# Kernel tuning notes

Hardware: AMD Instinct MI355X
Metric: run time of the kernel (lower is better)

## Reference

```python
import jax, jax.numpy as jnp
import numpy as np

STEP = 0.01  # matches init kwarg step=0.01


def _disc(x, step=STEP):
    """Discretize like pd.cut with bins arange(floor(min), ceil(max)+step, step).
    Bin identity is all that matters for entropy, so we return integer bin ids.
    (Boundary convention: half-open floor binning; pd.cut uses right-closed,
    which differs only on exact bin edges - measure-zero for continuous data.)"""
    lower = jnp.floor(jnp.min(x))
    return jnp.floor((x - lower) / step).astype(jnp.int32)


def _row_joint_entropy(labels_list):
    """Per-row empirical (joint) entropy in nats of discrete label tuples.
    H_row = -sum_v p_v log p_v = -(1/n) * sum_i log(count(x_i)/n),
    computed via pairwise-equality counts (vectorized Counter).
    labels_list: list of [B, n] int arrays. Returns [B]."""
    eq = None
    for lab in labels_list:
        e = lab[:, :, None] == lab[:, None, :]  # [B, n, n]
        eq = e if eq is None else (eq & e)
    n = labels_list[0].shape[1]
    counts = eq.sum(-1).astype(jnp.float32)  # [B, n]
    return -jnp.mean(jnp.log(counts / n), axis=-1)  # [B]


def _h_soft(o, d):
    """F.cross_entropy(o, softmax(d), 'mean') - F.kl_div(log_softmax(o), softmax(d), 'mean').
    Note torch kl_div 'mean' averages over ALL elements (B*C)."""
    p = jax.nn.softmax(d, axis=-1)
    logq = jax.nn.log_softmax(o, axis=-1)
    ce = -jnp.mean(jnp.sum(p * logq, axis=-1))          # mean over batch
    kl = jnp.mean(p * (jnp.log(p) - logq))               # mean over B*C
    return ce - kl


def reference(data, data1, data2, data3, output1, output2, output3, output):
    # --- reconstruction term ---
    mse_loss = 0.5 * jnp.mean((data - output) ** 2)

    # --- discrete entropies on detached inputs (torch: .detach().numpy()) ---
    d1 = _disc(jax.lax.stop_gradient(data1))
    d2 = _disc(jax.lax.stop_gradient(data2))
    d3 = _disc(jax.lax.stop_gradient(data3))

    H_data_1 = jnp.mean(_row_joint_entropy([d1]))
    H_data_2 = jnp.mean(_row_joint_entropy([d2]))
    H_data_3 = jnp.mean(_row_joint_entropy([d3]))

    H_output_1 = _h_soft(output1, data1)
    H_output_2 = _h_soft(output2, data2)
    H_output_3 = _h_soft(output3, data3)

    H_1 = H_data_1 - H_output_1
    H_2 = H_data_2 - H_output_2
    H_3 = H_data_3 - H_output_3

    # equal widths -> pad_matrices is a no-op
    H_in_1_3 = jnp.mean(_row_joint_entropy([d1, d3]))
    H_in_2_3 = jnp.mean(_row_joint_entropy([d2, d3]))
    H_in_1_2 = jnp.mean(_row_joint_entropy([d1, d2]))

    in1_3 = jnp.concatenate((data1, data3), axis=1)
    in2_3 = jnp.concatenate((data2, data3), axis=1)
    in1_2 = jnp.concatenate((data1, data2), axis=1)
    out1_3 = jnp.concatenate((output1, output3), axis=1)
    out2_3 = jnp.concatenate((output2, output3), axis=1)
    out1_2 = jnp.concatenate((output1, output2), axis=1)

    H_out_1_3 = _h_soft(out1_3, in1_3)
    H_out_2_3 = _h_soft(out2_3, in2_3)
    H_out_1_2 = _h_soft(out1_2, in1_2)

    data1_3 = H_data_1 + H_data_3 - H_in_1_3
    data2_3 = H_data_2 + H_data_3 - H_in_2_3
    data1_2 = H_data_1 + H_data_2 - H_in_1_2
    label1_3 = H_output_1 + H_output_3 - H_out_1_3
    label2_3 = H_output_2 + H_output_3 - H_out_2_3
    label1_2 = H_output_1 + H_output_2 - H_out_1_2

    H_MI1_3 = label1_3 - data1_3
    H_MI2_3 = label2_3 - data2_3
    H_MI1_2 = label1_2 - data1_2

    # per-row conditional MI I(X1; X2 | X3) = H(X1,X3)+H(X2,X3)-H(X3)-H(X1,X2,X3),
    # summed over rows (torch loop accumulates cmi per row without averaging)
    cmi_rows = (_row_joint_entropy([d1, d3]) + _row_joint_entropy([d2, d3])
                - _row_joint_entropy([d3]) - _row_joint_entropy([d1, d2, d3]))
    ave_data_ConMI = jnp.sum(cmi_rows)

    in123 = jnp.concatenate((data1, data2, data3), axis=1)
    out123 = jnp.concatenate((output1, output2, output3), axis=1)
    H_output_123 = _h_soft(out123, in123)
    ave_label_ConMI = H_out_2_3 - H_output_3 + H_out_1_3 - H_output_123
    CMI = ave_label_ConMI - ave_data_ConMI

    return (0.5 * mse_loss
            + 0.25 * (jnp.square(H_1) + jnp.square(H_2) + jnp.square(H_3))
            + 0.25 * (jnp.square(H_MI1_3) + jnp.square(H_MI2_3)
                      + jnp.square(H_MI1_2) + jnp.square(CMI)))


def setup_inputs() -> dict:
    key = jax.random.key(0)
    ks = jax.random.split(key, 8)
    B, D, DT = 2048, 256, 768
    return {
        "data": jax.random.normal(ks[0], (B, DT), dtype=jnp.float32),
        "data1": jax.random.normal(ks[1], (B, D), dtype=jnp.float32),
        "data2": jax.random.normal(ks[2], (B, D), dtype=jnp.float32),
        "data3": jax.random.normal(ks[3], (B, D), dtype=jnp.float32),
        "output1": jax.random.normal(ks[4], (B, D), dtype=jnp.float32),
        "output2": jax.random.normal(ks[5], (B, D), dtype=jnp.float32),
        "output3": jax.random.normal(ks[6], (B, D), dtype=jnp.float32),
        "output": jax.random.normal(ks[7], (B, DT), dtype=jnp.float32),
    }
```

## Files before the change

kernel.cpp:

```cpp
#include <hip/hip_runtime.h>
#include <math.h>

#define B_ROWS 2048
#define NCOL   256
#define DTOT   768
#define BANKS  16
#define HSLOTS 512
#define WPB    4
#define NBLK   (B_ROWS / WPB)


#define LO (-6.0f)

__global__ void zero_kernel(double* __restrict__ acc, unsigned int* __restrict__ ticket) {
    const int i = threadIdx.x;
    for (int z = i; z < BANKS * 22; z += 256) acc[z] = 0.0;
    if (i == 0) __hip_atomic_store(ticket, 0u, __ATOMIC_RELAXED, __HIP_MEMORY_SCOPE_AGENT);
}

__device__ __forceinline__ int hslot0(unsigned key) {
    return (int)((key * 0x9E3779B1u) >> 23);
}

__device__ __forceinline__ int hfix(unsigned* __restrict__ h, int slot,
                                    unsigned key, unsigned prev) {
    while (true) {
        if (prev == 0u) return slot;
        if ((prev >> 10) == key) { atomicAdd(&h[slot], 1u); return slot; }
        slot = (slot + 1) & (HSLOTS - 1);
        prev = atomicCAS(&h[slot], 0u, (key << 10) + 1u);
    }
}

__global__ __launch_bounds__(256)
void row_kernel(const float* __restrict__ d1, const float* __restrict__ d2,
                const float* __restrict__ d3,
                const float* __restrict__ o1, const float* __restrict__ o2,
                const float* __restrict__ o3,
                const float* __restrict__ data, const float* __restrict__ outp,
                double* __restrict__ acc, unsigned int* __restrict__ ticket,
                float* __restrict__ out) {
    __shared__ unsigned ht[WPB][7][HSLOTS];
    __shared__ float wlog[WPB][7];
    __shared__ float wce[WPB][7], wkl[WPB][7];
    __shared__ float wms[WPB];
    __shared__ float fin[22];
    __shared__ int   lastf;
    __shared__ double T[22];

    const int b = blockIdx.x, i = threadIdx.x;
    const int lane = i & 63, w = i >> 6;
    const int r = b * WPB + w;

    {
        unsigned* h = &ht[0][0][0];
        for (int z = i; z < WPB * 7 * HSLOTS; z += 256) h[z] = 0u;
    }

    float ms = 0.f;
    #pragma unroll
    for (int t = 0; t < WPB * 3; ++t) {
        const int idx = (b * WPB) * DTOT + t * 256 + i;
        const float dv = data[idx] - outp[idx];
        ms += dv * dv;
    }
    __syncthreads();

    const float4 X1 = ((const float4*)(d1 + r * NCOL))[lane];
    const float4 X2 = ((const float4*)(d2 + r * NCOL))[lane];
    const float4 X3 = ((const float4*)(d3 + r * NCOL))[lane];
    const float4 Y1 = ((const float4*)(o1 + r * NCOL))[lane];
    const float4 Y2 = ((const float4*)(o2 + r * NCOL))[lane];
    const float4 Y3 = ((const float4*)(o3 + r * NCOL))[lane];
    const float x1[4] = {X1.x, X1.y, X1.z, X1.w};
    const float x2[4] = {X2.x, X2.y, X2.z, X2.w};
    const float x3[4] = {X3.x, X3.y, X3.z, X3.w};
    const float y1[4] = {Y1.x, Y1.y, Y1.z, Y1.w};
    const float y2[4] = {Y2.x, Y2.y, Y2.z, Y2.w};
    const float y3[4] = {Y3.x, Y3.y, Y3.z, Y3.w};

    unsigned* t0 = ht[w][0]; unsigned* t1 = ht[w][1]; unsigned* t2 = ht[w][2];
    unsigned* t3 = ht[w][3]; unsigned* t4 = ht[w][4]; unsigned* t5 = ht[w][5];
    unsigned* t6 = ht[w][6];

    int sl[4][7];
    float sv[12] = {0,0,0,0,0,0,0,0,0,0,0,0};

    #pragma unroll
    for (int j = 0; j < 4; ++j) {
        const int m1 = (int)floorf((x1[j] - LO) / 0.01f);
        const int m2 = (int)floorf((x2[j] - LO) / 0.01f);
        const int m3 = (int)floorf((x3[j] - LO) / 0.01f);
        const unsigned k1 = (unsigned)m1, k2 = (unsigned)m2, k3 = (unsigned)m3;
        const unsigned k13 = k1 | (k3 << 11), k23 = k2 | (k3 << 11), k12 = k1 | (k2 << 11);
        int s1 = hslot0(k1), s2 = hslot0(k2), s3 = hslot0(k3);
        int s13 = hslot0(k13), s23 = hslot0(k23), s12 = hslot0(k12);
        const unsigned p1  = atomicCAS(&t0[s1],  0u, (k1  << 10) + 1u);
        const unsigned p2  = atomicCAS(&t1[s2],  0u, (k2  << 10) + 1u);
        const unsigned p3  = atomicCAS(&t2[s3],  0u, (k3  << 10) + 1u);
        const unsigned p13 = atomicCAS(&t3[s13], 0u, (k13 << 10) + 1u);
        const unsigned p23 = atomicCAS(&t4[s23], 0u, (k23 << 10) + 1u);
        const unsigned p12 = atomicCAS(&t5[s12], 0u, (k12 << 10) + 1u);
        sl[j][0] = hfix(t0, s1,  k1,  p1);
        sl[j][1] = hfix(t1, s2,  k2,  p2);
        sl[j][2] = hfix(t2, s3,  k3,  p3);
        sl[j][3] = s13 = hfix(t3, s13, k13, p13);
        sl[j][4] = hfix(t4, s23, k23, p23);
        sl[j][5] = hfix(t5, s12, k12, p12);
        const unsigned k123 = (unsigned)s13 | (k2 << 9);
        int s123 = hslot0(k123);
        const unsigned p123 = atomicCAS(&t6[s123], 0u, (k123 << 10) + 1u);
        sl[j][6] = hfix(t6, s123, k123, p123);

        const float ed1 = expf(x1[j]), ed2 = expf(x2[j]), ed3 = expf(x3[j]);
        sv[0] += ed1; sv[1] += ed1 * y1[j]; sv[2]  += ed1 * x1[j]; sv[3]  += expf(y1[j]);
        sv[4] += ed2; sv[5] += ed2 * y2[j]; sv[6]  += ed2 * x2[j]; sv[7]  += expf(y2[j]);
        sv[8] += ed3; sv[9] += ed3 * y3[j]; sv[10] += ed3 * x3[j]; sv[11] += expf(y3[j]);
    }

    #pragma unroll
    for (int s = 0; s < 12; ++s) {
        float x = sv[s];
        for (int off = 32; off; off >>= 1) x += __shfl_xor(x, off);
        sv[s] = x;
    }

    float logacc[7] = {0,0,0,0,0,0,0};
    #pragma unroll
    for (int j = 0; j < 4; ++j) {
        logacc[0] += logf((float)(t0[sl[j][0]] & 1023u));
        logacc[1] += logf((float)(t1[sl[j][1]] & 1023u));
        logacc[2] += logf((float)(t2[sl[j][2]] & 1023u));
        logacc[3] += logf((float)(t3[sl[j][3]] & 1023u));
        logacc[4] += logf((float)(t4[sl[j][4]] & 1023u));
        logacc[5] += logf((float)(t5[sl[j][5]] & 1023u));
        logacc[6] += logf((float)(t6[sl[j][6]] & 1023u));
    }
    #pragma unroll
    for (int s = 0; s < 7; ++s) {
        float x = logacc[s];
        for (int off = 32; off; off >>= 1) x += __shfl_down(x, off);
        if (lane == 0) wlog[w][s] = x;
    }

    if (lane < 7) {
        const int masks[7] = {1, 2, 4, 5, 6, 3, 7};
        const int mk = masks[lane];
        float Zd = 0.f, Td = 0.f, Ud = 0.f, Zo = 0.f;
        #pragma unroll
        for (int k = 0; k < 3; ++k)
            if ((mk >> k) & 1) { Zd += sv[4*k]; Td += sv[4*k+1]; Ud += sv[4*k+2]; Zo += sv[4*k+3]; }
        const float Ld = logf(Zd), Lo = logf(Zo);
        const float Spo = Td / Zd, Spd = Ud / Zd;
        wce[w][lane] = Lo - Spo;
        wkl[w][lane] = (Spd - Ld) - (Spo - Lo);
    }

    {
        float x = ms;
        for (int off = 32; off; off >>= 1) x += __shfl_down(x, off);
        if (lane == 0) wms[w] = x;
    }
    __syncthreads();

    if (i < 7)              fin[i]      = wlog[0][i] + wlog[1][i] + wlog[2][i] + wlog[3][i];
    else if (i < 14)        fin[i]      = wce[0][i-7] + wce[1][i-7] + wce[2][i-7] + wce[3][i-7];
    else if (i < 21)        fin[i]      = wkl[0][i-14] + wkl[1][i-14] + wkl[2][i-14] + wkl[3][i-14];
    else if (i == 21)       fin[21]     = wms[0] + wms[1] + wms[2] + wms[3];
    __syncthreads();
    if (i < 22) atomicAdd(&acc[(b & (BANKS - 1)) * 22 + i], (double)fin[i]);
    __syncthreads();
    if (i == 0) {
        const unsigned old = atomicAdd(ticket, 1u);
        lastf = (old == (unsigned)(NBLK - 1));
    }
    __syncthreads();

    if (lastf) {
        __threadfence();
        if (i < 22) {
            double s = 0.0;
            for (int bk = 0; bk < BANKS; ++bk)
                s += __hip_atomic_load(&acc[bk * 22 + i], __ATOMIC_RELAXED,
                                       __HIP_MEMORY_SCOPE_AGENT);
            T[i] = s;
        }
        __syncthreads();
        if (i == 0) {
            const double n = 256.0, Bd = 2048.0;
            const double logn = log(n);
            const double S1 = T[0], S2 = T[1], S3 = T[2];
            const double S13 = T[3], S23 = T[4], S12 = T[5], S123 = T[6];
            const double Hd1   = logn - S1  / (Bd * n);
            const double Hd2   = logn - S2  / (Bd * n);
            const double Hd3   = logn - S3  / (Bd * n);
            const double Hin13 = logn - S13 / (Bd * n);
            const double Hin23 = logn - S23 / (Bd * n);
            const double Hin12 = logn - S12 / (Bd * n);
            const double C[7] = {256, 256, 256, 512, 512, 512, 768};
            double Ho[7];
            for (int m = 0; m < 7; ++m) Ho[m] = T[7 + m] / Bd - T[14 + m] / (Bd * C[m]);
            const double H1 = Hd1 - Ho[0], H2 = Hd2 - Ho[1], H3 = Hd3 - Ho[2];
            const double MI13 = (Ho[0] + Ho[2] - Ho[3]) - (Hd1 + Hd3 - Hin13);
            const double MI23 = (Ho[1] + Ho[2] - Ho[4]) - (Hd2 + Hd3 - Hin23);
            const double MI12 = (Ho[0] + Ho[1] - Ho[5]) - (Hd1 + Hd2 - Hin12);
            const double aveD = -(S13 + S23 - S3 - S123) / n;
            const double aveL = Ho[4] - Ho[2] + Ho[3] - Ho[6];
            const double CMI = aveL - aveD;
            const double mse = 0.5 * T[21] / (Bd * 768.0);
            out[0] = (float)(0.5 * mse
                           + 0.25 * (H1 * H1 + H2 * H2 + H3 * H3)
                           + 0.25 * (MI13 * MI13 + MI23 * MI23 + MI12 * MI12
                                     + CMI * CMI));
        }
    }
}

extern "C" void kernel_launch(void* const* d_in, const int* in_sizes, int n_in,
                              void* d_out, int out_size, void* d_ws, size_t ws_size,
                              hipStream_t stream) {
    const float* data = (const float*)d_in[0];
    const float* d1   = (const float*)d_in[1];
    const float* d2   = (const float*)d_in[2];
    const float* d3   = (const float*)d_in[3];
    const float* o1   = (const float*)d_in[4];
    const float* o2   = (const float*)d_in[5];
    const float* o3   = (const float*)d_in[6];
    const float* outp = (const float*)d_in[7];

    double* acc          = (double*)((char*)d_ws + 768);
    unsigned int* ticket = (unsigned int*)((char*)d_ws + 3584);

    zero_kernel<<<1, 256, 0, stream>>>(acc, ticket);
    row_kernel<<<NBLK, 256, 0, stream>>>(d1, d2, d3, o1, o2, o3, data, outp,
                                         acc, ticket, (float*)d_out);
}
```

Baseline: 109.3 us.

## Replace atomic ticket reduction with per-block partials and separate fold kernel

Drops the zero kernel and the global double atomics plus last-block ticket. Each block now writes its 22 partial sums to a workspace array, and a single 512-thread fold kernel reduces them and computes the loss. Several other changes come with it: MSE loads are vectorized as float4, the shared hash table is zeroed with uint4 stores, wave reductions use DPP row ops plus readlane, fast __expf/__logf intrinsics replace expf/logf, and the hash-table CAS operations are batched per stage to raise memory-level parallelism. The fast math intrinsics lower precision, and the fold kernel is a serial single-block tail.

```diff
diff --git a/kernel.cpp b/kernel.cpp
--- a/kernel.cpp
+++ b/kernel.cpp
@@ -4,19 +4,12 @@
 #define B_ROWS 2048
 #define NCOL   256
 #define DTOT   768
-#define BANKS  16
 #define HSLOTS 512
 #define WPB    4
 #define NBLK   (B_ROWS / WPB)
 
 
 #define LO (-6.0f)
-
-__global__ void zero_kernel(double* __restrict__ acc, unsigned int* __restrict__ ticket) {
-    const int i = threadIdx.x;
-    for (int z = i; z < BANKS * 22; z += 256) acc[z] = 0.0;
-    if (i == 0) __hip_atomic_store(ticket, 0u, __ATOMIC_RELAXED, __HIP_MEMORY_SCOPE_AGENT);
-}
 
 __device__ __forceinline__ int hslot0(unsigned key) {
     return (int)((key * 0x9E3779B1u) >> 23);
@@ -32,37 +25,45 @@
     }
 }
 
+__device__ __forceinline__ float wave_red_sum(float x) {
+    int t;
+    t = __builtin_amdgcn_mov_dpp(__float_as_int(x), 0x111, 0xF, 0xF, true); x += __int_as_float(t);
+    t = __builtin_amdgcn_mov_dpp(__float_as_int(x), 0x112, 0xF, 0xF, true); x += __int_as_float(t);
+    t = __builtin_amdgcn_mov_dpp(__float_as_int(x), 0x114, 0xF, 0xF, true); x += __int_as_float(t);
+    t = __builtin_amdgcn_mov_dpp(__float_as_int(x), 0x118, 0xF, 0xF, true); x += __int_as_float(t);
+    t = __builtin_amdgcn_mov_dpp(__float_as_int(x), 0x142, 0xF, 0xF, true); x += __int_as_float(t);
+    t = __builtin_amdgcn_mov_dpp(__float_as_int(x), 0x143, 0xF, 0xF, true); x += __int_as_float(t);
+    return __int_as_float(__builtin_amdgcn_readlane(__float_as_int(x), 63));
+}
+
 __global__ __launch_bounds__(256)
 void row_kernel(const float* __restrict__ d1, const float* __restrict__ d2,
                 const float* __restrict__ d3,
                 const float* __restrict__ o1, const float* __restrict__ o2,
                 const float* __restrict__ o3,
                 const float* __restrict__ data, const float* __restrict__ outp,
-                double* __restrict__ acc, unsigned int* __restrict__ ticket,
-                float* __restrict__ out) {
+                double* __restrict__ part) {
     __shared__ unsigned ht[WPB][7][HSLOTS];
-    __shared__ float wlog[WPB][7];
-    __shared__ float wce[WPB][7], wkl[WPB][7];
-    __shared__ float wms[WPB];
-    __shared__ float fin[22];
-    __shared__ int   lastf;
-    __shared__ double T[22];
+    __shared__ float wlog[WPB][8];
+    __shared__ float wckl[WPB][14];
 
     const int b = blockIdx.x, i = threadIdx.x;
     const int lane = i & 63, w = i >> 6;
     const int r = b * WPB + w;
 
     {
-        unsigned* h = &ht[0][0][0];
-        for (int z = i; z < WPB * 7 * HSLOTS; z += 256) h[z] = 0u;
+        uint4* h4 = (uint4*)&ht[0][0][0];
+        #pragma unroll
+        for (int z = 0; z < 14; ++z) h4[i + z * 256] = make_uint4(0u, 0u, 0u, 0u);
     }
 
     float ms = 0.f;
     #pragma unroll
-    for (int t = 0; t < WPB * 3; ++t) {
-        const int idx = (b * WPB) * DTOT + t * 256 + i;
-        const float dv = data[idx] - outp[idx];
-        ms += dv * dv;
+    for (int t = 0; t < 3; ++t) {
+        const float4 a = ((const float4*)data)[b * 768 + t * 256 + i];
+        const float4 o = ((const float4*)outp)[b * 768 + t * 256 + i];
+        const float dx = a.x - o.x, dy = a.y - o.y, dz = a.z - o.z, dw = a.w - o.w;
+        ms += dx * dx + dy * dy + dz * dz + dw * dw;
     }
     __syncthreads();
 
@@ -83,136 +84,150 @@
     unsigned* t3 = ht[w][3]; unsigned* t4 = ht[w][4]; unsigned* t5 = ht[w][5];
     unsigned* t6 = ht[w][6];
 
-    int sl[4][7];
+    unsigned K1[4], K2[4], K3[4], K13[4], K23[4], K12[4];
+    int S1[4], S2[4], S3[4], S13[4], S23[4], S12[4];
+    unsigned P1[4], P2[4], P3[4], P13[4], P23[4], P12[4];
+    #pragma unroll
+    for (int j = 0; j < 4; ++j) {
+        K1[j] = (unsigned)(int)floorf((x1[j] - LO) / 0.01f);
+        K2[j] = (unsigned)(int)floorf((x2[j] - LO) / 0.01f);
+        K3[j] = (unsigned)(int)floorf((x3[j] - LO) / 0.01f);
+        K13[j] = K1[j] | (K3[j] << 11);
+        K23[j] = K2[j] | (K3[j] << 11);
+        K12[j] = K1[j] | (K2[j] << 11);
+        S1[j] = hslot0(K1[j]);   S2[j] = hslot0(K2[j]);   S3[j] = hslot0(K3[j]);
+        S13[j] = hslot0(K13[j]); S23[j] = hslot0(K23[j]); S12[j] = hslot0(K12[j]);
+    }
+    #pragma unroll
+    for (int j = 0; j < 4; ++j) {
+        P1[j]  = atomicCAS(&t0[S1[j]],  0u, (K1[j]  << 10) + 1u);
+        P2[j]  = atomicCAS(&t1[S2[j]],  0u, (K2[j]  << 10) + 1u);
+        P3[j]  = atomicCAS(&t2[S3[j]],  0u, (K3[j]  << 10) + 1u);
+        P13[j] = atomicCAS(&t3[S13[j]], 0u, (K13[j] << 10) + 1u);
+        P23[j] = atomicCAS(&t4[S23[j]], 0u, (K23[j] << 10) + 1u);
+        P12[j] = atomicCAS(&t5[S12[j]], 0u, (K12[j] << 10) + 1u);
+    }
+    #pragma unroll
+    for (int j = 0; j < 4; ++j) {
+        S1[j]  = hfix(t0, S1[j],  K1[j],  P1[j]);
+        S2[j]  = hfix(t1, S2[j],  K2[j],  P2[j]);
+        S3[j]  = hfix(t2, S3[j],  K3[j],  P3[j]);
+        S13[j] = hfix(t3, S13[j], K13[j], P13[j]);
+        S23[j] = hfix(t4, S23[j], K23[j], P23[j]);
+        S12[j] = hfix(t5, S12[j], K12[j], P12[j]);
+    }
+    unsigned K123[4], P123[4]; int S123[4];
+    #pragma unroll
+    for (int j = 0; j < 4; ++j) {
+        K123[j] = (unsigned)S123[j >= 0 ? 0 : 0];
+        K123[j] = (unsigned)S13[j] | (K2[j] << 9);
+        S123[j] = hslot0(K123[j]);
+        P123[j] = atomicCAS(&t6[S123[j]], 0u, (K123[j] << 10) + 1u);
+    }
+    #pragma unroll
+    for (int j = 0; j < 4; ++j) S123[j] = hfix(t6, S123[j], K123[j], P123[j]);
+
     float sv[12] = {0,0,0,0,0,0,0,0,0,0,0,0};
-
-    #pragma unroll
-    for (int j = 0; j < 4; ++j) {
-        const int m1 = (int)floorf((x1[j] - LO) / 0.01f);
-        const int m2 = (int)floorf((x2[j] - LO) / 0.01f);
-        const int m3 = (int)floorf((x3[j] - LO) / 0.01f);
-        const unsigned k1 = (unsigned)m1, k2 = (unsigned)m2, k3 = (unsigned)m3;
-        const unsigned k13 = k1 | (k3 << 11), k23 = k2 | (k3 << 11), k12 = k1 | (k2 << 11);
-        int s1 = hslot0(k1), s2 = hslot0(k2), s3 = hslot0(k3);
-        int s13 = hslot0(k13), s23 = hslot0(k23), s12 = hslot0(k12);
-        const unsigned p1  = atomicCAS(&t0[s1],  0u, (k1  << 10) + 1u);
-        const unsigned p2  = atomicCAS(&t1[s2],  0u, (k2  << 10) + 1u);
-        const unsigned p3  = atomicCAS(&t2[s3],  0u, (k3  << 10) + 1u);
-        const unsigned p13 = atomicCAS(&t3[s13], 0u, (k13 << 10) + 1u);
-        const unsigned p23 = atomicCAS(&t4[s23], 0u, (k23 << 10) + 1u);
-        const unsigned p12 = atomicCAS(&t5[s12], 0u, (k12 << 10) + 1u);
-        sl[j][0] = hfix(t0, s1,  k1,  p1);
-        sl[j][1] = hfix(t1, s2,  k2,  p2);
-        sl[j][2] = hfix(t2, s3,  k3,  p3);
-        sl[j][3] = s13 = hfix(t3, s13, k13, p13);
-        sl[j][4] = hfix(t4, s23, k23, p23);
-        sl[j][5] = hfix(t5, s12, k12, p12);
-        const unsigned k123 = (unsigned)s13 | (k2 << 9);
-        int s123 = hslot0(k123);
-        const unsigned p123 = atomicCAS(&t6[s123], 0u, (k123 << 10) + 1u);
-        sl[j][6] = hfix(t6, s123, k123, p123);
-
-        const float ed1 = expf(x1[j]), ed2 = expf(x2[j]), ed3 = expf(x3[j]);
-        sv[0] += ed1; sv[1] += ed1 * y1[j]; sv[2]  += ed1 * x1[j]; sv[3]  += expf(y1[j]);
-        sv[4] += ed2; sv[5] += ed2 * y2[j]; sv[6]  += ed2 * x2[j]; sv[7]  += expf(y2[j]);
-        sv[8] += ed3; sv[9] += ed3 * y3[j]; sv[10] += ed3 * x3[j]; sv[11] += expf(y3[j]);
-    }
-
-    #pragma unroll
-    for (int s = 0; s < 12; ++s) {
-        float x = sv[s];
-        for (int off = 32; off; off >>= 1) x += __shfl_xor(x, off);
-        sv[s] = x;
+    #pragma unroll
+    for (int j = 0; j < 4; ++j) {
+        const float ed1 = __expf(x1[j]), ed2 = __expf(x2[j]), ed3 = __expf(x3[j]);
+        sv[0] += ed1; sv[1] += ed1 * y1[j]; sv[2]  += ed1 * x1[j]; sv[3]  += __expf(y1[j]);
+        sv[4] += ed2; sv[5] += ed2 * y2[j]; sv[6]  += ed2 * x2[j]; sv[7]  += __expf(y2[j]);
+        sv[8] += ed3; sv[9] += ed3 * y3[j]; sv[10] += ed3 * x3[j]; sv[11] += __expf(y3[j]);
     }
 
     float logacc[7] = {0,0,0,0,0,0,0};
     #pragma unroll
     for (int j = 0; j < 4; ++j) {
-        logacc[0] += logf((float)(t0[sl[j][0]] & 1023u));
-        logacc[1] += logf((float)(t1[sl[j][1]] & 1023u));
-        logacc[2] += logf((float)(t2[sl[j][2]] & 1023u));
-        logacc[3] += logf((float)(t3[sl[j][3]] & 1023u));
-        logacc[4] += logf((float)(t4[sl[j][4]] & 1023u));
-        logacc[5] += logf((float)(t5[sl[j][5]] & 1023u));
-        logacc[6] += logf((float)(t6[sl[j][6]] & 1023u));
-    }
-    #pragma unroll
-    for (int s = 0; s < 7; ++s) {
-        float x = logacc[s];
-        for (int off = 32; off; off >>= 1) x += __shfl_down(x, off);
-        if (lane == 0) wlog[w][s] = x;
-    }
-
+        logacc[0] += __logf((float)(t0[S1[j]]   & 1023u));
+        logacc[1] += __logf((float)(t1[S2[j]]   & 1023u));
+        logacc[2] += __logf((float)(t2[S3[j]]   & 1023u));
+        logacc[3] += __logf((float)(t3[S13[j]]  & 1023u));
+        logacc[4] += __logf((float)(t4[S23[j]]  & 1023u));
+        logacc[5] += __logf((float)(t5[S12[j]]  & 1023u));
+        logacc[6] += __logf((float)(t6[S123[j]] & 1023u));
+    }
+
+    float svt[12];
+    #pragma unroll
+    for (int s = 0; s < 12; ++s) svt[s] = wave_red_sum(sv[s]);
+    float lgt[7];
+    #pragma unroll
+    for (int s = 0; s < 7; ++s) lgt[s] = wave_red_sum(logacc[s]);
+    const float mst = wave_red_sum(ms);
+
+    if (lane == 0) {
+        #pragma unroll
+        for (int s = 0; s < 7; ++s) wlog[w][s] = lgt[s];
+        wlog[w][7] = mst;
+    }
     if (lane < 7) {
         const int masks[7] = {1, 2, 4, 5, 6, 3, 7};
         const int mk = masks[lane];
         float Zd = 0.f, Td = 0.f, Ud = 0.f, Zo = 0.f;
         #pragma unroll
         for (int k = 0; k < 3; ++k)
-            if ((mk >> k) & 1) { Zd += sv[4*k]; Td += sv[4*k+1]; Ud += sv[4*k+2]; Zo += sv[4*k+3]; }
-        const float Ld = logf(Zd), Lo = logf(Zo);
+            if ((mk >> k) & 1) { Zd += svt[4*k]; Td += svt[4*k+1]; Ud += svt[4*k+2]; Zo += svt[4*k+3]; }
+        const float Ld = __logf(Zd), Lo = __logf(Zo);
         const float Spo = Td / Zd, Spd = Ud / Zd;
-        wce[w][lane] = Lo - Spo;
-        wkl[w][lane] = (Spd - Ld) - (Spo - Lo);
-    }
-
-    {
-        float x = ms;
-        for (int off = 32; off; off >>= 1) x += __shfl_down(x, off);
-        if (lane == 0) wms[w] = x;
+        wckl[w][lane]     = Lo - Spo;
+        wckl[w][7 + lane] = (Spd - Ld) - (Spo - Lo);
     }
     __syncthreads();
 
-    if (i < 7)              fin[i]      = wlog[0][i] + wlog[1][i] + wlog[2][i] + wlog[3][i];
-    else if (i < 14)        fin[i]      = wce[0][i-7] + wce[1][i-7] + wce[2][i-7] + wce[3][i-7];
-    else if (i < 21)        fin[i]      = wkl[0][i-14] + wkl[1][i-14] + wkl[2][i-14] + wkl[3][i-14];
-    else if (i == 21)       fin[21]     = wms[0] + wms[1] + wms[2] + wms[3];
-    __syncthreads();
-    if (i < 22) atomicAdd(&acc[(b & (BANKS - 1)) * 22 + i], (double)fin[i]);
-    __syncthreads();
-    if (i == 0) {
-        const unsigned old = atomicAdd(ticket, 1u);
-        lastf = (old == (unsigned)(NBLK - 1));
-    }
-    __syncthreads();
-
-    if (lastf) {
-        __threadfence();
-        if (i < 22) {
+    if (i < 22) {
+        float f;
+        if (i < 7)        f = wlog[0][i] + wlog[1][i] + wlog[2][i] + wlog[3][i];
+        else if (i < 14)  f = wckl[0][i-7] + wckl[1][i-7] + wckl[2][i-7] + wckl[3][i-7];
+        else if (i < 21)  f = wckl[0][i-7] + wckl[1][i-7] + wckl[2][i-7] + wckl[3][i-7];
+        else              f = wlog[0][7] + wlog[1][7] + wlog[2][7] + wlog[3][7];
+        part[i * NBLK + b] = (double)f;
+    }
+}
+
+__global__ __launch_bounds__(512)
+void fold_kernel(const double* __restrict__ part, float* __restrict__ out) {
+    __shared__ double ws8[8];
+    __shared__ double T[22];
+    const int i = threadIdx.x, lane = i & 63, w = i >> 6;
+    for (int j = 0; j < 22; ++j) {
+        double v = part[j * NBLK + i];
+        for (int off = 32; off; off >>= 1) v += __shfl_down(v, off);
+        if (lane == 0) ws8[w] = v;
+        __syncthreads();
+        if (i == 0) {
             double s = 0.0;
-            for (int bk = 0; bk < BANKS; ++bk)
-                s += __hip_atomic_load(&acc[bk * 22 + i], __ATOMIC_RELAXED,
-                                       __HIP_MEMORY_SCOPE_AGENT);
-            T[i] = s;
+            for (int k = 0; k < 8; ++k) s += ws8[k];
+            T[j] = s;
         }
         __syncthreads();
-        if (i == 0) {
-            const double n = 256.0, Bd = 2048.0;
-            const double logn = log(n);
-            const double S1 = T[0], S2 = T[1], S3 = T[2];
-            const double S13 = T[3], S23 = T[4], S12 = T[5], S123 = T[6];
-            const double Hd1   = logn - S1  / (Bd * n);
-            const double Hd2   = logn - S2  / (Bd * n);
-            const double Hd3   = logn - S3  / (Bd * n);
-            const double Hin13 = logn - S13 / (Bd * n);
-            const double Hin23 = logn - S23 / (Bd * n);
-            const double Hin12 = logn - S12 / (Bd * n);
-            const double C[7] = {256, 256, 256, 512, 512, 512, 768};
-            double Ho[7];
-            for (int m = 0; m < 7; ++m) Ho[m] = T[7 + m] / Bd - T[14 + m] / (Bd * C[m]);
-            const double H1 = Hd1 - Ho[0], H2 = Hd2 - Ho[1], H3 = Hd3 - Ho[2];
-            const double MI13 = (Ho[0] + Ho[2] - Ho[3]) - (Hd1 + Hd3 - Hin13);
-            const double MI23 = (Ho[1] + Ho[2] - Ho[4]) - (Hd2 + Hd3 - Hin23);
-            const double MI12 = (Ho[0] + Ho[1] - Ho[5]) - (Hd1 + Hd2 - Hin12);
-            const double aveD = -(S13 + S23 - S3 - S123) / n;
-            const double aveL = Ho[4] - Ho[2] + Ho[3] - Ho[6];
-            const double CMI = aveL - aveD;
-            const double mse = 0.5 * T[21] / (Bd * 768.0);
-            out[0] = (float)(0.5 * mse
-                           + 0.25 * (H1 * H1 + H2 * H2 + H3 * H3)
-                           + 0.25 * (MI13 * MI13 + MI23 * MI23 + MI12 * MI12
-                                     + CMI * CMI));
-        }
+    }
+    if (i == 0) {
+        const double n = 256.0, Bd = 2048.0;
+        const double logn = log(n);
+        const double S1 = T[0], S2 = T[1], S3 = T[2];
+        const double S13 = T[3], S23 = T[4], S12 = T[5], S123 = T[6];
+        const double Hd1   = logn - S1  / (Bd * n);
+        const double Hd2   = logn - S2  / (Bd * n);
+        const double Hd3   = logn - S3  / (Bd * n);
+        const double Hin13 = logn - S13 / (Bd * n);
+        const double Hin23 = logn - S23 / (Bd * n);
+        const double Hin12 = logn - S12 / (Bd * n);
+        const double C[7] = {256, 256, 256, 512, 512, 512, 768};
+        double Ho[7];
+        for (int m = 0; m < 7; ++m) Ho[m] = T[7 + m] / Bd - T[14 + m] / (Bd * C[m]);
+        const double H1 = Hd1 - Ho[0], H2 = Hd2 - Ho[1], H3 = Hd3 - Ho[2];
+        const double MI13 = (Ho[0] + Ho[2] - Ho[3]) - (Hd1 + Hd3 - Hin13);
+        const double MI23 = (Ho[1] + Ho[2] - Ho[4]) - (Hd2 + Hd3 - Hin23);
+        const double MI12 = (Ho[0] + Ho[1] - Ho[5]) - (Hd1 + Hd2 - Hin12);
+        const double aveD = -(S13 + S23 - S3 - S123) / n;
+        const double aveL = Ho[4] - Ho[2] + Ho[3] - Ho[6];
+        const double CMI = aveL - aveD;
+        const double mse = 0.5 * T[21] / (Bd * 768.0);
+        out[0] = (float)(0.5 * mse
+                       + 0.25 * (H1 * H1 + H2 * H2 + H3 * H3)
+                       + 0.25 * (MI13 * MI13 + MI23 * MI23 + MI12 * MI12
+                                 + CMI * CMI));
     }
 }
 
@@ -228,10 +243,8 @@
     const float* o3   = (const float*)d_in[6];
     const float* outp = (const float*)d_in[7];
 
-    double* acc          = (double*)((char*)d_ws + 768);
-    unsigned int* ticket = (unsigned int*)((char*)d_ws + 3584);
-
-    zero_kernel<<<1, 256, 0, stream>>>(acc, ticket);
-    row_kernel<<<NBLK, 256, 0, stream>>>(d1, d2, d3, o1, o2, o3, data, outp,
-                                         acc, ticket, (float*)d_out);
-}
+    double* part = (double*)d_ws;
+
+    row_kernel<<<NBLK, 256, 0, stream>>>(d1, d2, d3, o1, o2, o3, data, outp, part);
+    fold_kernel<<<1, 512, 0, stream>>>(part, (float*)d_out);
+}
```

New measurement: 119.8 us. +9.6%, slower.
